# Kernel optimization log

Measured on AMD Instinct MI355X. Metric: run time of the kernel, lower is better.

The kernel has to match this reference:

```python
import jax, jax.numpy as jnp
import numpy as np
from jax import lax

N, E, F_NODE, F_EDGE, H, L = 100000, 3200000, 5, 2, 32, 18


def setup_inputs() -> dict:
    key = jax.random.key(0)
    ks = jax.random.split(key, 20)
    s = 0.1
    return {
        "x": jax.random.normal(ks[0], (N, F_NODE), dtype=jnp.float32),
        "edge_attr": jax.random.uniform(ks[1], (E, F_EDGE), dtype=jnp.float32),
        "edge_index": jax.random.randint(ks[2], (2, E), 0, N, dtype=jnp.int32),
        "Wn": jax.random.normal(ks[3], (F_NODE, H), dtype=jnp.float32) * s,
        "bn": jnp.zeros((H,), jnp.float32),
        "We": jax.random.normal(ks[4], (F_EDGE, H), dtype=jnp.float32) * s,
        "be": jnp.zeros((H,), jnp.float32),
        "ln_w": jax.random.normal(ks[5], (L, H, H), dtype=jnp.float32) * s,
        "ln_b": jnp.zeros((L, H), jnp.float32),
        "le_w": jax.random.normal(ks[6], (L, H, H), dtype=jnp.float32) * s,
        "le_b": jnp.zeros((L, H), jnp.float32),
        "lu_w": jax.random.normal(ks[7], (L, 2 * H, H), dtype=jnp.float32) * s,
        "lu_b": jnp.zeros((L, H), jnp.float32),
        "c1_w": jax.random.normal(ks[8], (H, H), dtype=jnp.float32) * s,
        "c1_b": jnp.zeros((H,), jnp.float32),
        "c2_w": jax.random.normal(ks[9], (H, 1), dtype=jnp.float32) * s,
        "c2_b": jnp.zeros((1,), jnp.float32),
    }


def reference(x, edge_attr, edge_index, Wn, bn, We, be,
              ln_w, ln_b, le_w, le_b, lu_w, lu_b, c1_w, c1_b, c2_w, c2_b):
    src, dst = edge_index[0], edge_index[1]
    n = x.shape[0]
    h = x @ Wn + bn                       # [N, H] node encoder
    ea = edge_attr @ We + be              # [E, H] edge encoder (shared by all layers)

    def layer(h, p):
        lnw, lnb, lew, leb, luw, lub = p
        ee = ea @ lew + leb               # [E, H] per-layer edge embedding
        xj = h[src]                       # gather source node states [E, H]
        msg = xj * (1.0 - ee) + ee * (xj @ lnw + lnb)
        agg = jax.ops.segment_sum(msg, dst, num_segments=n)  # scatter-add [N, H]
        out = jnp.concatenate([h, agg], axis=1) @ luw + lub
        return jax.nn.relu(out), None

    h, _ = lax.scan(layer, h, (ln_w, ln_b, le_w, le_b, lu_w, lu_b))
    logits = jax.nn.relu(h @ c1_w + c1_b) @ c2_w + c2_b   # classifier (dropout off at eval)
    return jax.nn.sigmoid(logits).squeeze(-1)             # [N]
```

## Files before the change

kernel.cpp:

```cpp
#include <hip/hip_runtime.h>
#include <hip/hip_bf16.h>
#include <hip/hip_fp8.h>
#include <math.h>

#define H 32
#define SCB 1024
#define S 6

__device__ __forceinline__ unsigned f2bf(float f) {
  unsigned u = __float_as_uint(f);
  return (u + 0x7fffu + ((u >> 16) & 1u)) >> 16;
}
__device__ __forceinline__ float bflo(unsigned p) { return __uint_as_float(p << 16); }
__device__ __forceinline__ float bfhi(unsigned p) { return __uint_as_float(p & 0xffff0000u); }

__device__ __forceinline__ unsigned f2q(float f) {
  __hip_fp8_e4m3 q(f);
  return (unsigned)q.__x;
}
__device__ __forceinline__ float q2f(unsigned b) {
  unsigned s = (b >> 7) & 1u, e = (b >> 3) & 15u, m = b & 7u;
  float vn = __uint_as_float((s << 31) | ((e + 120u) << 23) | (m << 20));
  float vs = __uint_as_float((s << 31) | 0x3f800000u) * ((float)(int)m * (1.0f / 512.0f));
  return (e == 0u) ? vs : vn;
}

template <bool HI>
__device__ __forceinline__ void cvt2(unsigned dw, float& x, float& u) {
#if __has_builtin(__builtin_amdgcn_cvt_pk_f32_fp8)
  typedef float f32x2 __attribute__((ext_vector_type(2)));
  f32x2 v = __builtin_amdgcn_cvt_pk_f32_fp8((int)dw, HI);
  x = v[0]; u = v[1];
#else
  unsigned b = HI ? (dw >> 16) : dw;
  x = q2f(b & 255u); u = q2f((b >> 8) & 255u);
#endif
}

__device__ __forceinline__ unsigned pack4(float x0, float u0, float x1, float u1) {
  return f2q(x0) | (f2q(u0) << 8) | (f2q(x1) << 16) | (f2q(u1) << 24);
}

__global__ void k_encode(const float* __restrict__ x, const float* __restrict__ Wn,
                         const float* __restrict__ bn, const float* __restrict__ lnw0,
                         const float* __restrict__ lnb0, float* __restrict__ h,
                         unsigned* __restrict__ pk, int n, int fnode) {
  __shared__ float sw[H * H];
  int tid = threadIdx.x;
  for (int i = tid; i < H * H; i += blockDim.x) sw[i] = lnw0[i];
  __syncthreads();
  int gid = blockIdx.x * blockDim.x + tid;
  int node = gid >> 5, c = gid & 31;
  if (node >= n) return;
  float acc = bn[c];
  for (int k = 0; k < fnode; ++k)
    acc = fmaf(x[node * fnode + k], Wn[k * H + c], acc);
  h[node * H + c] = acc;
  float t = lnb0[c];
#pragma unroll
  for (int k = 0; k < H; ++k)
    t = fmaf(__shfl(acc, k, 32), sw[k * H + c], t);
  unsigned w = f2q(acc) | (f2q(t - acc) << 8);
  unsigned dw = w | (__shfl_xor(w, 1, 32) << 16);
  if (!(c & 1)) pk[node * 16 + (c >> 1)] = dw;
}

__global__ void k_fold(const float* __restrict__ We, const float* __restrict__ be,
                       const float* __restrict__ lew, const float* __restrict__ leb,
                       float* __restrict__ W2, float* __restrict__ b2, int L) {
  int gid = blockIdx.x * blockDim.x + threadIdx.x;
  if (gid >= L * H) return;
  int l = gid >> 5, c = gid & 31;
  const float* lw = lew + (size_t)l * H * H;
  float a0 = 0.f, a1 = 0.f, bb = leb[l * H + c];
  for (int j = 0; j < H; ++j) {
    float w = lw[j * H + c];
    a0 = fmaf(We[j], w, a0);
    a1 = fmaf(We[H + j], w, a1);
    bb = fmaf(be[j], w, bb);
  }
  W2[l * 2 * H + c] = a0;
  W2[l * 2 * H + H + c] = a1;
  b2[l * H + c] = bb;
}

__global__ void k_hist(const int* __restrict__ dst, unsigned* __restrict__ cnt, int e) {
  int i = blockIdx.x * blockDim.x + threadIdx.x;
  if (i < e) atomicAdd(&cnt[dst[i]], 1u);
}

__global__ void k_scan1(const unsigned* __restrict__ cnt, unsigned* __restrict__ out,
                        unsigned* __restrict__ bsum, int n) {
  __shared__ unsigned s[SCB];
  int i = blockIdx.x * SCB + threadIdx.x;
  unsigned v = (i < n) ? cnt[i] : 0u;
  s[threadIdx.x] = v;
  __syncthreads();
  for (int off = 1; off < SCB; off <<= 1) {
    unsigned u = (threadIdx.x >= off) ? s[threadIdx.x - off] : 0u;
    __syncthreads();
    s[threadIdx.x] += u;
    __syncthreads();
  }
  if (i < n) out[i] = s[threadIdx.x] - v;
  if (threadIdx.x == SCB - 1) bsum[blockIdx.x] = s[SCB - 1];
}

__global__ void k_scan2(const unsigned* __restrict__ bsum, unsigned* __restrict__ boff,
                        unsigned* __restrict__ total_out, int nb) {
  __shared__ unsigned s[SCB];
  unsigned v = ((int)threadIdx.x < nb) ? bsum[threadIdx.x] : 0u;
  s[threadIdx.x] = v;
  __syncthreads();
  for (int off = 1; off < SCB; off <<= 1) {
    unsigned u = (threadIdx.x >= off) ? s[threadIdx.x - off] : 0u;
    __syncthreads();
    s[threadIdx.x] += u;
    __syncthreads();
  }
  if ((int)threadIdx.x < nb) boff[threadIdx.x] = s[threadIdx.x] - v;
  if (threadIdx.x == SCB - 1) *total_out = s[SCB - 1];
}

__global__ void k_scan3(unsigned* __restrict__ row_ptr, const unsigned* __restrict__ boff,
                        unsigned* __restrict__ fill, int n) {
  int i = blockIdx.x * blockDim.x + threadIdx.x;
  if (i >= n) return;
  unsigned v = row_ptr[i] + boff[i >> 10];
  row_ptr[i] = v;
  fill[i] = v;
}

__global__ void k_scatter(const int* __restrict__ src, const int* __restrict__ dst,
                          const float* __restrict__ ea, unsigned* __restrict__ fill,
                          unsigned long long* __restrict__ recs, int e) {
  int i = blockIdx.x * blockDim.x + threadIdx.x;
  if (i >= e) return;
  int d = dst[i];
  unsigned pos = atomicAdd(&fill[d], 1u);
  float2 a = ((const float2*)ea)[i];
  unsigned long long v = (unsigned long long)(unsigned)src[i] |
                         ((unsigned long long)(f2bf(a.x) | (f2bf(a.y) << 16)) << 32);
  __builtin_nontemporal_store(v, &recs[pos]);
}

__device__ __forceinline__ void edge_acc(float (&acc)[8], uint4 pv, unsigned attr, float v,
                                         const float (&w0v)[8], const float (&w1v)[8],
                                         const float (&bbv)[8]) {
  float a0 = bflo(attr), a1 = bfhi(attr);
  unsigned dws[4] = {pv.x, pv.y, pv.z, pv.w};
#pragma unroll
  for (int d = 0; d < 4; ++d) {
    float x0, u0, x1, u1;
    cvt2<false>(dws[d], x0, u0);
    cvt2<true>(dws[d], x1, u1);
    float e0 = fmaf(a0, w0v[2 * d], fmaf(a1, w1v[2 * d], bbv[2 * d]));
    float e1 = fmaf(a0, w0v[2 * d + 1], fmaf(a1, w1v[2 * d + 1], bbv[2 * d + 1]));
    acc[2 * d]     = fmaf(v, fmaf(e0, u0, x0), acc[2 * d]);
    acc[2 * d + 1] = fmaf(v, fmaf(e1, u1, x1), acc[2 * d + 1]);
  }
}

__global__ void __launch_bounds__(256) k_gather(
    const unsigned* __restrict__ pk, const unsigned* __restrict__ row_ptr,
    const unsigned long long* __restrict__ recs, const float* __restrict__ W2l,
    const float* __restrict__ b2l, float* __restrict__ agg, int n, int e) {
  int tid = threadIdx.x;
  int lane = tid & 63;
  int wv = blockIdx.x * 4 + (tid >> 6);
  int n0 = wv * S;
  if (n0 >= n) return;
  int sub = lane & 3;
  unsigned eoff = (unsigned)(lane >> 2);
  float w0v[8], w1v[8], bbv[8];
#pragma unroll
  for (int j = 0; j < 8; ++j) {
    int ch = sub * 8 + j;
    w0v[j] = W2l[ch]; w1v[j] = W2l[H + ch]; bbv[j] = b2l[ch];
  }
  unsigned rp[S + 1];
#pragma unroll
  for (int i = 0; i <= S; ++i) {
    int idx = n0 + i;
    rp[i] = row_ptr[idx < n ? idx : n];
  }
  unsigned b0[S], b1[S], rr[S];
  unsigned R = 0;
#pragma unroll
  for (int s = 0; s < S; ++s) {
    b0[s] = rp[s]; b1[s] = rp[s + 1];
    rr[s] = (b1[s] - b0[s] + 15u) >> 4;
    R = rr[s] > R ? rr[s] : R;
  }
  float acc[S][8] = {};
  const uint4* pk4 = (const uint4*)pk;
  unsigned emax = (unsigned)(e - 1);
  unsigned long long cur[S], nxt[S];
#pragma unroll
  for (int s = 0; s < S; ++s) {
    unsigned ix = b0[s] + eoff;
    unsigned cl = (ix < b1[s]) ? ix : b0[s];
    cl = cl < emax ? cl : emax;
    cur[s] = __builtin_nontemporal_load(&recs[cl]);
  }
  for (unsigned r = 0; r < R; ++r) {
    uint4 pv[S];
#pragma unroll
    for (int s = 0; s < S; ++s)
      if (r < rr[s]) pv[s] = pk4[(size_t)(unsigned)cur[s] * 4 + sub];
#pragma unroll
    for (int s = 0; s < S; ++s) {
      nxt[s] = cur[s];
      if (r + 1 < rr[s]) {
        unsigned ix = b0[s] + (r + 1) * 16u + eoff;
        unsigned cl = (ix < b1[s]) ? ix : b0[s];
        cl = cl < emax ? cl : emax;
        nxt[s] = __builtin_nontemporal_load(&recs[cl]);
      }
    }
    unsigned rb = r << 4;
#pragma unroll
    for (int s = 0; s < S; ++s)
      if (r < rr[s]) {
        float v = (b0[s] + rb + eoff < b1[s]) ? 1.f : 0.f;
        edge_acc(acc[s], pv[s], (unsigned)(cur[s] >> 32), v, w0v, w1v, bbv);
      }
#pragma unroll
    for (int s = 0; s < S; ++s) cur[s] = nxt[s];
  }
#pragma unroll
  for (int s = 0; s < S; ++s)
#pragma unroll
    for (int j = 0; j < 8; ++j) {
      acc[s][j] += __shfl_xor(acc[s][j], 4, 64);
      acc[s][j] += __shfl_xor(acc[s][j], 8, 64);
      acc[s][j] += __shfl_xor(acc[s][j], 16, 64);
      acc[s][j] += __shfl_xor(acc[s][j], 32, 64);
    }
  if (lane < 4) {
#pragma unroll
    for (int s = 0; s < S; ++s) {
      if (n0 + s < n) {
        float4* o = (float4*)&agg[(size_t)(n0 + s) * H + lane * 8];
        o[0] = make_float4(acc[s][0], acc[s][1], acc[s][2], acc[s][3]);
        o[1] = make_float4(acc[s][4], acc[s][5], acc[s][6], acc[s][7]);
      }
    }
  }
}

__global__ void __launch_bounds__(256) k_update(
    const float* __restrict__ h, const float* __restrict__ agg,
    const float* __restrict__ luw, const float* __restrict__ lub,
    const float* __restrict__ lnw, const float* __restrict__ lnb,
    float* __restrict__ hout, unsigned* __restrict__ pkout, int n) {
  int node = blockIdx.x * blockDim.x + threadIdx.x;
  if (node >= n) return;
  float hr[H], ar[H];
  const float4* h4 = (const float4*)(h + (size_t)node * H);
  const float4* a4 = (const float4*)(agg + (size_t)node * H);
#pragma unroll
  for (int q = 0; q < 8; ++q) {
    float4 v = h4[q];
    hr[4 * q] = v.x; hr[4 * q + 1] = v.y; hr[4 * q + 2] = v.z; hr[4 * q + 3] = v.w;
  }
#pragma unroll
  for (int q = 0; q < 8; ++q) {
    float4 v = a4[q];
    ar[4 * q] = v.x; ar[4 * q + 1] = v.y; ar[4 * q + 2] = v.z; ar[4 * q + 3] = v.w;
  }
  float o[H];
#pragma unroll
  for (int c = 0; c < H; ++c) o[c] = lub[c];
#pragma unroll
  for (int k = 0; k < H; ++k)
#pragma unroll
    for (int c = 0; c < H; ++c)
      o[c] = fmaf(hr[k], luw[k * H + c], o[c]);
#pragma unroll
  for (int k = 0; k < H; ++k)
#pragma unroll
    for (int c = 0; c < H; ++c)
      o[c] = fmaf(ar[k], luw[(H + k) * H + c], o[c]);
#pragma unroll
  for (int c = 0; c < H; ++c) o[c] = fmaxf(o[c], 0.f);
  float4* ho = (float4*)(hout + (size_t)node * H);
#pragma unroll
  for (int q = 0; q < 8; ++q)
    ho[q] = make_float4(o[4 * q], o[4 * q + 1], o[4 * q + 2], o[4 * q + 3]);
  if (pkout) {
    float t[H];
#pragma unroll
    for (int c = 0; c < H; ++c) t[c] = lnb[c];
#pragma unroll
    for (int k = 0; k < H; ++k)
#pragma unroll
      for (int c = 0; c < H; ++c)
        t[c] = fmaf(o[k], lnw[k * H + c], t[c]);
    unsigned dws[16];
#pragma unroll
    for (int d = 0; d < 16; ++d)
      dws[d] = pack4(o[2 * d], t[2 * d] - o[2 * d],
                     o[2 * d + 1], t[2 * d + 1] - o[2 * d + 1]);
    uint4* po = (uint4*)(pkout + (size_t)node * 16);
#pragma unroll
    for (int q = 0; q < 4; ++q)
      po[q] = make_uint4(dws[4 * q], dws[4 * q + 1], dws[4 * q + 2], dws[4 * q + 3]);
  }
}

__global__ void k_cls(const float* __restrict__ h, const float* __restrict__ c1w,
                      const float* __restrict__ c1b, const float* __restrict__ c2w,
                      const float* __restrict__ c2b, float* __restrict__ out, int n) {
  __shared__ float sw[H * H];
  int tid = threadIdx.x;
  for (int i = tid; i < H * H; i += blockDim.x) sw[i] = c1w[i];
  __syncthreads();
  int gid = blockIdx.x * blockDim.x + tid;
  int node = gid >> 5, c = gid & 31;
  if (node >= n) return;
  float hv = h[node * H + c];
  float z = c1b[c];
#pragma unroll
  for (int k = 0; k < H; ++k)
    z = fmaf(__shfl(hv, k, 32), sw[k * H + c], z);
  z = fmaxf(z, 0.f);
  float r = z * c2w[c];
#pragma unroll
  for (int m = 16; m >= 1; m >>= 1)
    r += __shfl_xor(r, m, 32);
  if (c == 0) out[node] = 1.f / (1.f + expf(-(r + c2b[0])));
}

extern "C" void kernel_launch(void* const* d_in, const int* in_sizes, int n_in,
                              void* d_out, int out_size, void* d_ws, size_t ws_size,
                              hipStream_t stream) {
  const float* x         = (const float*)d_in[0];
  const float* edge_attr = (const float*)d_in[1];
  const int*   edge_index= (const int*)d_in[2];
  const float* Wn        = (const float*)d_in[3];
  const float* bn        = (const float*)d_in[4];
  const float* We        = (const float*)d_in[5];
  const float* be        = (const float*)d_in[6];
  const float* ln_w      = (const float*)d_in[7];
  const float* ln_b      = (const float*)d_in[8];
  const float* le_w      = (const float*)d_in[9];
  const float* le_b      = (const float*)d_in[10];
  const float* lu_w      = (const float*)d_in[11];
  const float* lu_b      = (const float*)d_in[12];
  const float* c1w       = (const float*)d_in[13];
  const float* c1b       = (const float*)d_in[14];
  const float* c2w       = (const float*)d_in[15];
  const float* c2b       = (const float*)d_in[16];

  const int N_ = in_sizes[0] / 5;
  const int E_ = in_sizes[1] / 2;
  const int L_ = in_sizes[7] / (H * H);
  const int* src = edge_index;
  const int* dst = edge_index + E_;

  char* ws = (char*)d_ws;
  size_t off = 0;
  auto alloc = [&](size_t bytes) -> void* {
    void* p = ws + off;
    off = (off + bytes + 255) & ~(size_t)255;
    return p;
  };
  float*              hA      = (float*)alloc((size_t)N_ * H * 4);
  float*              hB      = (float*)alloc((size_t)N_ * H * 4);
  unsigned*           pkA     = (unsigned*)alloc((size_t)N_ * 16 * 4);
  unsigned*           pkB     = (unsigned*)alloc((size_t)N_ * 16 * 4);
  float*              agg     = (float*)alloc((size_t)N_ * H * 4);
  unsigned*           row_ptr = (unsigned*)alloc((size_t)(N_ + 1) * 4);
  unsigned*           fill    = (unsigned*)alloc((size_t)N_ * 4);
  unsigned long long* recs    = (unsigned long long*)alloc((size_t)E_ * 8);
  float*              W2      = (float*)alloc((size_t)L_ * 2 * H * 4);
  float*              b2      = (float*)alloc((size_t)L_ * H * 4);
  unsigned*           bsum    = (unsigned*)alloc((size_t)SCB * 4);
  unsigned*           boff    = (unsigned*)alloc((size_t)SCB * 4);

  const int tb = 256;
  const int nb = (N_ + SCB - 1) / SCB;
  hipMemsetAsync(fill, 0, (size_t)N_ * 4, stream);
  k_encode<<<(N_ * 32 + tb - 1) / tb, tb, 0, stream>>>(x, Wn, bn, ln_w, ln_b, hA, pkA, N_, 5);
  k_fold<<<(L_ * H + 63) / 64, 64, 0, stream>>>(We, be, le_w, le_b, W2, b2, L_);
  k_hist<<<(E_ + tb - 1) / tb, tb, 0, stream>>>(dst, fill, E_);
  k_scan1<<<nb, SCB, 0, stream>>>(fill, row_ptr, bsum, N_);
  k_scan2<<<1, SCB, 0, stream>>>(bsum, boff, row_ptr + N_, nb);
  k_scan3<<<(N_ + tb - 1) / tb, tb, 0, stream>>>(row_ptr, boff, fill, N_);
  k_scatter<<<(E_ + tb - 1) / tb, tb, 0, stream>>>(src, dst, edge_attr, fill, recs, E_);

  float* hc = hA;  float* hn = hB;
  unsigned* pc = pkA; unsigned* pn = pkB;
  const int gblocks = (N_ + 4 * S - 1) / (4 * S);
  for (int l = 0; l < L_; ++l) {
    bool last = (l == L_ - 1);
    k_gather<<<gblocks, 256, 0, stream>>>(
        pc, row_ptr, recs, W2 + l * 2 * H, b2 + l * H, agg, N_, E_);
    k_update<<<(N_ + tb - 1) / tb, tb, 0, stream>>>(
        hc, agg, lu_w + (size_t)l * 2 * H * H, lu_b + (size_t)l * H,
        last ? nullptr : ln_w + (size_t)(l + 1) * H * H,
        last ? nullptr : ln_b + (size_t)(l + 1) * H,
        hn, last ? nullptr : pn, N_);
    float* tf = hc; hc = hn; hn = tf;
    unsigned* tp = pc; pc = pn; pn = tp;
  }
  k_cls<<<(N_ * 32 + tb - 1) / tb, tb, 0, stream>>>(hc, c1w, c1b, c2w, c2b, (float*)d_out, N_);
}
```

Baseline: 2.260 ms.

## Partition CSR scatter by XCD and deepen gather prefetch pipeline

The CSR scatter kernel becomes a persistent kernel in which each block reads its XCC hardware ID and first handles destination ranges owned by its own XCD. Chunks are handed out through per-range atomic work queues, so the atomics and record writes for a destination range tend to stay in one XCD's L2 instead of bouncing across dies. The gather kernel gets a two-deep prefetch of edge records and one-ahead prefetch of packed node features, with fewer nodes per wave (S 6→4) to offset the extra registers, and it drops the nontemporal hints. The cost is that each edge chunk's dst array is re-read 8 times in the scatter, and the gather uses more registers per node slot.

```diff
diff --git a/kernel.cpp b/kernel.cpp
--- a/kernel.cpp
+++ b/kernel.cpp
@@ -5,7 +5,9 @@
 
 #define H 32
 #define SCB 1024
-#define S 6
+#define S 4
+#define NXCD 8
+#define SCCH 4096
 
 __device__ __forceinline__ unsigned f2bf(float f) {
   unsigned u = __float_as_uint(f);
@@ -131,17 +133,37 @@
   fill[i] = v;
 }
 
-__global__ void k_scatter(const int* __restrict__ src, const int* __restrict__ dst,
-                          const float* __restrict__ ea, unsigned* __restrict__ fill,
-                          unsigned long long* __restrict__ recs, int e) {
-  int i = blockIdx.x * blockDim.x + threadIdx.x;
-  if (i >= e) return;
-  int d = dst[i];
-  unsigned pos = atomicAdd(&fill[d], 1u);
-  float2 a = ((const float2*)ea)[i];
-  unsigned long long v = (unsigned long long)(unsigned)src[i] |
-                         ((unsigned long long)(f2bf(a.x) | (f2bf(a.y) << 16)) << 32);
-  __builtin_nontemporal_store(v, &recs[pos]);
+__global__ void __launch_bounds__(256) k_scatter(
+    const int* __restrict__ src, const int* __restrict__ dst,
+    const float* __restrict__ ea, unsigned* __restrict__ fill,
+    uint2* __restrict__ recs, unsigned* __restrict__ q, int e, int n) {
+  __shared__ unsigned sh_chunk;
+  unsigned xcc;
+  asm volatile("s_getreg_b32 %0, hwreg(HW_REG_XCC_ID)" : "=s"(xcc));
+  xcc &= (NXCD - 1);
+  const unsigned nchunks = (unsigned)((e + SCCH - 1) / SCCH);
+  for (int pass = 0; pass < NXCD; ++pass) {
+    unsigned qi = (xcc + (unsigned)pass) & (NXCD - 1);
+    unsigned lo = (unsigned)((unsigned long long)n * qi / NXCD);
+    unsigned hi = (unsigned)((unsigned long long)n * (qi + 1) / NXCD);
+    for (;;) {
+      if (threadIdx.x == 0) sh_chunk = atomicAdd(&q[qi], 1u);
+      __syncthreads();
+      unsigned c = sh_chunk;
+      __syncthreads();
+      if (c >= nchunks) break;
+      int base = (int)(c * SCCH);
+      int end = base + SCCH; end = end < e ? end : e;
+      for (int i = base + (int)threadIdx.x; i < end; i += 256) {
+        unsigned d = (unsigned)dst[i];
+        if (d >= lo && d < hi) {
+          unsigned pos = atomicAdd(&fill[d], 1u);
+          float2 a = ((const float2*)ea)[i];
+          recs[pos] = make_uint2((unsigned)src[i], f2bf(a.x) | (f2bf(a.y) << 16));
+        }
+      }
+    }
+  }
 }
 
 __device__ __forceinline__ void edge_acc(float (&acc)[8], uint4 pv, unsigned attr, float v,
@@ -163,7 +185,7 @@
 
 __global__ void __launch_bounds__(256) k_gather(
     const unsigned* __restrict__ pk, const unsigned* __restrict__ row_ptr,
-    const unsigned long long* __restrict__ recs, const float* __restrict__ W2l,
+    const uint2* __restrict__ recs, const float* __restrict__ W2l,
     const float* __restrict__ b2l, float* __restrict__ agg, int n, int e) {
   int tid = threadIdx.x;
   int lane = tid & 63;
@@ -195,27 +217,39 @@
   float acc[S][8] = {};
   const uint4* pk4 = (const uint4*)pk;
   unsigned emax = (unsigned)(e - 1);
-  unsigned long long cur[S], nxt[S];
+  uint2 cur[S], nxt[S];
+  uint4 pcur[S];
 #pragma unroll
   for (int s = 0; s < S; ++s) {
     unsigned ix = b0[s] + eoff;
     unsigned cl = (ix < b1[s]) ? ix : b0[s];
-    cl = cl < emax ? cl : emax;
-    cur[s] = __builtin_nontemporal_load(&recs[cl]);
-  }
+    cur[s] = recs[cl < emax ? cl : emax];
+  }
+#pragma unroll
+  for (int s = 0; s < S; ++s) {
+    nxt[s] = cur[s];
+    if (rr[s] > 1) {
+      unsigned ix = b0[s] + 16u + eoff;
+      unsigned cl = (ix < b1[s]) ? ix : b0[s];
+      nxt[s] = recs[cl < emax ? cl : emax];
+    }
+  }
+#pragma unroll
+  for (int s = 0; s < S; ++s)
+    if (rr[s] > 0) pcur[s] = pk4[(size_t)cur[s].x * 4 + sub];
   for (unsigned r = 0; r < R; ++r) {
-    uint4 pv[S];
+    uint4 pnxt[S];
 #pragma unroll
     for (int s = 0; s < S; ++s)
-      if (r < rr[s]) pv[s] = pk4[(size_t)(unsigned)cur[s] * 4 + sub];
+      if (r + 1 < rr[s]) pnxt[s] = pk4[(size_t)nxt[s].x * 4 + sub];
+    uint2 fut[S];
 #pragma unroll
     for (int s = 0; s < S; ++s) {
-      nxt[s] = cur[s];
-      if (r + 1 < rr[s]) {
-        unsigned ix = b0[s] + (r + 1) * 16u + eoff;
+      fut[s] = nxt[s];
+      if (r + 2 < rr[s]) {
+        unsigned ix = b0[s] + (r + 2) * 16u + eoff;
         unsigned cl = (ix < b1[s]) ? ix : b0[s];
-        cl = cl < emax ? cl : emax;
-        nxt[s] = __builtin_nontemporal_load(&recs[cl]);
+        fut[s] = recs[cl < emax ? cl : emax];
       }
     }
     unsigned rb = r << 4;
@@ -223,10 +257,12 @@
     for (int s = 0; s < S; ++s)
       if (r < rr[s]) {
         float v = (b0[s] + rb + eoff < b1[s]) ? 1.f : 0.f;
-        edge_acc(acc[s], pv[s], (unsigned)(cur[s] >> 32), v, w0v, w1v, bbv);
+        edge_acc(acc[s], pcur[s], cur[s].y, v, w0v, w1v, bbv);
       }
 #pragma unroll
-    for (int s = 0; s < S; ++s) cur[s] = nxt[s];
+    for (int s = 0; s < S; ++s) {
+      cur[s] = nxt[s]; nxt[s] = fut[s]; pcur[s] = pnxt[s];
+    }
   }
 #pragma unroll
   for (int s = 0; s < S; ++s)
@@ -366,29 +402,31 @@
     off = (off + bytes + 255) & ~(size_t)255;
     return p;
   };
-  float*              hA      = (float*)alloc((size_t)N_ * H * 4);
-  float*              hB      = (float*)alloc((size_t)N_ * H * 4);
-  unsigned*           pkA     = (unsigned*)alloc((size_t)N_ * 16 * 4);
-  unsigned*           pkB     = (unsigned*)alloc((size_t)N_ * 16 * 4);
-  float*              agg     = (float*)alloc((size_t)N_ * H * 4);
-  unsigned*           row_ptr = (unsigned*)alloc((size_t)(N_ + 1) * 4);
-  unsigned*           fill    = (unsigned*)alloc((size_t)N_ * 4);
-  unsigned long long* recs    = (unsigned long long*)alloc((size_t)E_ * 8);
-  float*              W2      = (float*)alloc((size_t)L_ * 2 * H * 4);
-  float*              b2      = (float*)alloc((size_t)L_ * H * 4);
-  unsigned*           bsum    = (unsigned*)alloc((size_t)SCB * 4);
-  unsigned*           boff    = (unsigned*)alloc((size_t)SCB * 4);
+  float*    hA      = (float*)alloc((size_t)N_ * H * 4);
+  float*    hB      = (float*)alloc((size_t)N_ * H * 4);
+  unsigned* pkA     = (unsigned*)alloc((size_t)N_ * 16 * 4);
+  unsigned* pkB     = (unsigned*)alloc((size_t)N_ * 16 * 4);
+  float*    agg     = (float*)alloc((size_t)N_ * H * 4);
+  unsigned* row_ptr = (unsigned*)alloc((size_t)(N_ + 1) * 4);
+  unsigned* fill    = (unsigned*)alloc((size_t)N_ * 4);
+  uint2*    recs    = (uint2*)alloc((size_t)E_ * 8);
+  float*    W2      = (float*)alloc((size_t)L_ * 2 * H * 4);
+  float*    b2      = (float*)alloc((size_t)L_ * H * 4);
+  unsigned* bsum    = (unsigned*)alloc((size_t)SCB * 4);
+  unsigned* boff    = (unsigned*)alloc((size_t)SCB * 4);
+  unsigned* qq      = (unsigned*)alloc((size_t)NXCD * 4);
 
   const int tb = 256;
   const int nb = (N_ + SCB - 1) / SCB;
   hipMemsetAsync(fill, 0, (size_t)N_ * 4, stream);
+  hipMemsetAsync(qq, 0, (size_t)NXCD * 4, stream);
   k_encode<<<(N_ * 32 + tb - 1) / tb, tb, 0, stream>>>(x, Wn, bn, ln_w, ln_b, hA, pkA, N_, 5);
   k_fold<<<(L_ * H + 63) / 64, 64, 0, stream>>>(We, be, le_w, le_b, W2, b2, L_);
   k_hist<<<(E_ + tb - 1) / tb, tb, 0, stream>>>(dst, fill, E_);
   k_scan1<<<nb, SCB, 0, stream>>>(fill, row_ptr, bsum, N_);
   k_scan2<<<1, SCB, 0, stream>>>(bsum, boff, row_ptr + N_, nb);
   k_scan3<<<(N_ + tb - 1) / tb, tb, 0, stream>>>(row_ptr, boff, fill, N_);
-  k_scatter<<<(E_ + tb - 1) / tb, tb, 0, stream>>>(src, dst, edge_attr, fill, recs, E_);
+  k_scatter<<<1024, 256, 0, stream>>>(src, dst, edge_attr, fill, recs, qq, E_, N_);
 
   float* hc = hA;  float* hn = hB;
   unsigned* pc = pkA; unsigned* pn = pkB;
```

Result: faster. 2.176 ms (-3.7%).

## Split packed node features into two channel halves gathered in separate passes

Applied to the files above, without the earlier changes.

The packed fp8 node table is stored as two half-width arrays of 16 channels each, and each layer runs the gather kernel twice, once per half. Each half-table is 3.2MB instead of 6.4MB, so a pass is more likely to stay in cache during the random source gathers. The cost is reading the edge records twice per layer and launching an extra kernel. Nodes per wave drop from 6 to 4, and the edge records lose their nontemporal load and store hints, so they may now stay cached between the two passes.

```diff
diff --git a/kernel.cpp b/kernel.cpp
--- a/kernel.cpp
+++ b/kernel.cpp
@@ -5,7 +5,7 @@
 
 #define H 32
 #define SCB 1024
-#define S 6
+#define S 4
 
 __device__ __forceinline__ unsigned f2bf(float f) {
   unsigned u = __float_as_uint(f);
@@ -44,7 +44,8 @@
 __global__ void k_encode(const float* __restrict__ x, const float* __restrict__ Wn,
                          const float* __restrict__ bn, const float* __restrict__ lnw0,
                          const float* __restrict__ lnb0, float* __restrict__ h,
-                         unsigned* __restrict__ pk, int n, int fnode) {
+                         unsigned* __restrict__ pk0, unsigned* __restrict__ pk1,
+                         int n, int fnode) {
   __shared__ float sw[H * H];
   int tid = threadIdx.x;
   for (int i = tid; i < H * H; i += blockDim.x) sw[i] = lnw0[i];
@@ -62,7 +63,10 @@
     t = fmaf(__shfl(acc, k, 32), sw[k * H + c], t);
   unsigned w = f2q(acc) | (f2q(t - acc) << 8);
   unsigned dw = w | (__shfl_xor(w, 1, 32) << 16);
-  if (!(c & 1)) pk[node * 16 + (c >> 1)] = dw;
+  if (!(c & 1)) {
+    unsigned* ph = (c < 16) ? pk0 : pk1;
+    ph[node * 8 + ((c & 15) >> 1)] = dw;
+  }
 }
 
 __global__ void k_fold(const float* __restrict__ We, const float* __restrict__ be,
@@ -133,15 +137,13 @@
 
 __global__ void k_scatter(const int* __restrict__ src, const int* __restrict__ dst,
                           const float* __restrict__ ea, unsigned* __restrict__ fill,
-                          unsigned long long* __restrict__ recs, int e) {
+                          uint2* __restrict__ recs, int e) {
   int i = blockIdx.x * blockDim.x + threadIdx.x;
   if (i >= e) return;
   int d = dst[i];
   unsigned pos = atomicAdd(&fill[d], 1u);
   float2 a = ((const float2*)ea)[i];
-  unsigned long long v = (unsigned long long)(unsigned)src[i] |
-                         ((unsigned long long)(f2bf(a.x) | (f2bf(a.y) << 16)) << 32);
-  __builtin_nontemporal_store(v, &recs[pos]);
+  recs[pos] = make_uint2((unsigned)src[i], f2bf(a.x) | (f2bf(a.y) << 16));
 }
 
 __device__ __forceinline__ void edge_acc(float (&acc)[8], uint4 pv, unsigned attr, float v,
@@ -162,20 +164,20 @@
 }
 
 __global__ void __launch_bounds__(256) k_gather(
-    const unsigned* __restrict__ pk, const unsigned* __restrict__ row_ptr,
-    const unsigned long long* __restrict__ recs, const float* __restrict__ W2l,
-    const float* __restrict__ b2l, float* __restrict__ agg, int n, int e) {
+    const unsigned* __restrict__ pkh, const unsigned* __restrict__ row_ptr,
+    const uint2* __restrict__ recs, const float* __restrict__ W2l,
+    const float* __restrict__ b2l, int co, float* __restrict__ agg, int n, int e) {
   int tid = threadIdx.x;
   int lane = tid & 63;
   int wv = blockIdx.x * 4 + (tid >> 6);
   int n0 = wv * S;
   if (n0 >= n) return;
-  int sub = lane & 3;
-  unsigned eoff = (unsigned)(lane >> 2);
+  int sub = lane & 1;
+  unsigned eoff = (unsigned)(lane >> 1);
   float w0v[8], w1v[8], bbv[8];
 #pragma unroll
   for (int j = 0; j < 8; ++j) {
-    int ch = sub * 8 + j;
+    int ch = co + sub * 8 + j;
     w0v[j] = W2l[ch]; w1v[j] = W2l[H + ch]; bbv[j] = b2l[ch];
   }
   unsigned rp[S + 1];
@@ -189,41 +191,39 @@
 #pragma unroll
   for (int s = 0; s < S; ++s) {
     b0[s] = rp[s]; b1[s] = rp[s + 1];
-    rr[s] = (b1[s] - b0[s] + 15u) >> 4;
+    rr[s] = (b1[s] - b0[s] + 31u) >> 5;
     R = rr[s] > R ? rr[s] : R;
   }
   float acc[S][8] = {};
-  const uint4* pk4 = (const uint4*)pk;
+  const uint4* pk4 = (const uint4*)pkh;
   unsigned emax = (unsigned)(e - 1);
-  unsigned long long cur[S], nxt[S];
+  uint2 cur[S], nxt[S];
 #pragma unroll
   for (int s = 0; s < S; ++s) {
     unsigned ix = b0[s] + eoff;
     unsigned cl = (ix < b1[s]) ? ix : b0[s];
-    cl = cl < emax ? cl : emax;
-    cur[s] = __builtin_nontemporal_load(&recs[cl]);
+    cur[s] = recs[cl < emax ? cl : emax];
   }
   for (unsigned r = 0; r < R; ++r) {
     uint4 pv[S];
 #pragma unroll
     for (int s = 0; s < S; ++s)
-      if (r < rr[s]) pv[s] = pk4[(size_t)(unsigned)cur[s] * 4 + sub];
+      if (r < rr[s]) pv[s] = pk4[(size_t)cur[s].x * 2 + sub];
 #pragma unroll
     for (int s = 0; s < S; ++s) {
       nxt[s] = cur[s];
       if (r + 1 < rr[s]) {
-        unsigned ix = b0[s] + (r + 1) * 16u + eoff;
+        unsigned ix = b0[s] + (r + 1) * 32u + eoff;
         unsigned cl = (ix < b1[s]) ? ix : b0[s];
-        cl = cl < emax ? cl : emax;
-        nxt[s] = __builtin_nontemporal_load(&recs[cl]);
+        nxt[s] = recs[cl < emax ? cl : emax];
       }
     }
-    unsigned rb = r << 4;
+    unsigned rb = r << 5;
 #pragma unroll
     for (int s = 0; s < S; ++s)
       if (r < rr[s]) {
         float v = (b0[s] + rb + eoff < b1[s]) ? 1.f : 0.f;
-        edge_acc(acc[s], pv[s], (unsigned)(cur[s] >> 32), v, w0v, w1v, bbv);
+        edge_acc(acc[s], pv[s], cur[s].y, v, w0v, w1v, bbv);
       }
 #pragma unroll
     for (int s = 0; s < S; ++s) cur[s] = nxt[s];
@@ -232,16 +232,17 @@
   for (int s = 0; s < S; ++s)
 #pragma unroll
     for (int j = 0; j < 8; ++j) {
+      acc[s][j] += __shfl_xor(acc[s][j], 2, 64);
       acc[s][j] += __shfl_xor(acc[s][j], 4, 64);
       acc[s][j] += __shfl_xor(acc[s][j], 8, 64);
       acc[s][j] += __shfl_xor(acc[s][j], 16, 64);
       acc[s][j] += __shfl_xor(acc[s][j], 32, 64);
     }
-  if (lane < 4) {
+  if (lane < 2) {
 #pragma unroll
     for (int s = 0; s < S; ++s) {
       if (n0 + s < n) {
-        float4* o = (float4*)&agg[(size_t)(n0 + s) * H + lane * 8];
+        float4* o = (float4*)&agg[(size_t)(n0 + s) * H + co + lane * 8];
         o[0] = make_float4(acc[s][0], acc[s][1], acc[s][2], acc[s][3]);
         o[1] = make_float4(acc[s][4], acc[s][5], acc[s][6], acc[s][7]);
       }
@@ -253,7 +254,8 @@
     const float* __restrict__ h, const float* __restrict__ agg,
     const float* __restrict__ luw, const float* __restrict__ lub,
     const float* __restrict__ lnw, const float* __restrict__ lnb,
-    float* __restrict__ hout, unsigned* __restrict__ pkout, int n) {
+    float* __restrict__ hout, unsigned* __restrict__ pk0,
+    unsigned* __restrict__ pk1, int n) {
   int node = blockIdx.x * blockDim.x + threadIdx.x;
   if (node >= n) return;
   float hr[H], ar[H];
@@ -288,7 +290,7 @@
 #pragma unroll
   for (int q = 0; q < 8; ++q)
     ho[q] = make_float4(o[4 * q], o[4 * q + 1], o[4 * q + 2], o[4 * q + 3]);
-  if (pkout) {
+  if (pk0) {
     float t[H];
 #pragma unroll
     for (int c = 0; c < H; ++c) t[c] = lnb[c];
@@ -302,10 +304,12 @@
     for (int d = 0; d < 16; ++d)
       dws[d] = pack4(o[2 * d], t[2 * d] - o[2 * d],
                      o[2 * d + 1], t[2 * d + 1] - o[2 * d + 1]);
-    uint4* po = (uint4*)(pkout + (size_t)node * 16);
-#pragma unroll
-    for (int q = 0; q < 4; ++q)
-      po[q] = make_uint4(dws[4 * q], dws[4 * q + 1], dws[4 * q + 2], dws[4 * q + 3]);
+    uint4* p0 = (uint4*)(pk0 + (size_t)node * 8);
+    p0[0] = make_uint4(dws[0], dws[1], dws[2], dws[3]);
+    p0[1] = make_uint4(dws[4], dws[5], dws[6], dws[7]);
+    uint4* p1 = (uint4*)(pk1 + (size_t)node * 8);
+    p1[0] = make_uint4(dws[8], dws[9], dws[10], dws[11]);
+    p1[1] = make_uint4(dws[12], dws[13], dws[14], dws[15]);
   }
 }
 
@@ -366,23 +370,25 @@
     off = (off + bytes + 255) & ~(size_t)255;
     return p;
   };
-  float*              hA      = (float*)alloc((size_t)N_ * H * 4);
-  float*              hB      = (float*)alloc((size_t)N_ * H * 4);
-  unsigned*           pkA     = (unsigned*)alloc((size_t)N_ * 16 * 4);
-  unsigned*           pkB     = (unsigned*)alloc((size_t)N_ * 16 * 4);
-  float*              agg     = (float*)alloc((size_t)N_ * H * 4);
-  unsigned*           row_ptr = (unsigned*)alloc((size_t)(N_ + 1) * 4);
-  unsigned*           fill    = (unsigned*)alloc((size_t)N_ * 4);
-  unsigned long long* recs    = (unsigned long long*)alloc((size_t)E_ * 8);
-  float*              W2      = (float*)alloc((size_t)L_ * 2 * H * 4);
-  float*              b2      = (float*)alloc((size_t)L_ * H * 4);
-  unsigned*           bsum    = (unsigned*)alloc((size_t)SCB * 4);
-  unsigned*           boff    = (unsigned*)alloc((size_t)SCB * 4);
+  float*    hA      = (float*)alloc((size_t)N_ * H * 4);
+  float*    hB      = (float*)alloc((size_t)N_ * H * 4);
+  unsigned* pkA0    = (unsigned*)alloc((size_t)N_ * 8 * 4);
+  unsigned* pkA1    = (unsigned*)alloc((size_t)N_ * 8 * 4);
+  unsigned* pkB0    = (unsigned*)alloc((size_t)N_ * 8 * 4);
+  unsigned* pkB1    = (unsigned*)alloc((size_t)N_ * 8 * 4);
+  float*    agg     = (float*)alloc((size_t)N_ * H * 4);
+  unsigned* row_ptr = (unsigned*)alloc((size_t)(N_ + 1) * 4);
+  unsigned* fill    = (unsigned*)alloc((size_t)N_ * 4);
+  uint2*    recs    = (uint2*)alloc((size_t)E_ * 8);
+  float*    W2      = (float*)alloc((size_t)L_ * 2 * H * 4);
+  float*    b2      = (float*)alloc((size_t)L_ * H * 4);
+  unsigned* bsum    = (unsigned*)alloc((size_t)SCB * 4);
+  unsigned* boff    = (unsigned*)alloc((size_t)SCB * 4);
 
   const int tb = 256;
   const int nb = (N_ + SCB - 1) / SCB;
   hipMemsetAsync(fill, 0, (size_t)N_ * 4, stream);
-  k_encode<<<(N_ * 32 + tb - 1) / tb, tb, 0, stream>>>(x, Wn, bn, ln_w, ln_b, hA, pkA, N_, 5);
+  k_encode<<<(N_ * 32 + tb - 1) / tb, tb, 0, stream>>>(x, Wn, bn, ln_w, ln_b, hA, pkA0, pkA1, N_, 5);
   k_fold<<<(L_ * H + 63) / 64, 64, 0, stream>>>(We, be, le_w, le_b, W2, b2, L_);
   k_hist<<<(E_ + tb - 1) / tb, tb, 0, stream>>>(dst, fill, E_);
   k_scan1<<<nb, SCB, 0, stream>>>(fill, row_ptr, bsum, N_);
@@ -391,19 +397,23 @@
   k_scatter<<<(E_ + tb - 1) / tb, tb, 0, stream>>>(src, dst, edge_attr, fill, recs, E_);
 
   float* hc = hA;  float* hn = hB;
-  unsigned* pc = pkA; unsigned* pn = pkB;
+  unsigned* pc0 = pkA0; unsigned* pc1 = pkA1;
+  unsigned* pn0 = pkB0; unsigned* pn1 = pkB1;
   const int gblocks = (N_ + 4 * S - 1) / (4 * S);
   for (int l = 0; l < L_; ++l) {
     bool last = (l == L_ - 1);
-    k_gather<<<gblocks, 256, 0, stream>>>(
-        pc, row_ptr, recs, W2 + l * 2 * H, b2 + l * H, agg, N_, E_);
+    const float* w2l = W2 + l * 2 * H;
+    const float* b2l = b2 + l * H;
+    k_gather<<<gblocks, 256, 0, stream>>>(pc0, row_ptr, recs, w2l, b2l, 0, agg, N_, E_);
+    k_gather<<<gblocks, 256, 0, stream>>>(pc1, row_ptr, recs, w2l, b2l, 16, agg, N_, E_);
     k_update<<<(N_ + tb - 1) / tb, tb, 0, stream>>>(
         hc, agg, lu_w + (size_t)l * 2 * H * H, lu_b + (size_t)l * H,
         last ? nullptr : ln_w + (size_t)(l + 1) * H * H,
         last ? nullptr : ln_b + (size_t)(l + 1) * H,
-        hn, last ? nullptr : pn, N_);
+        hn, last ? nullptr : pn0, last ? nullptr : pn1, N_);
     float* tf = hc; hc = hn; hn = tf;
-    unsigned* tp = pc; pc = pn; pn = tp;
+    unsigned* t0 = pc0; pc0 = pn0; pn0 = t0;
+    unsigned* t1 = pc1; pc1 = pn1; pn1 = t1;
   }
   k_cls<<<(N_ * 32 + tb - 1) / tb, tb, 0, stream>>>(hc, c1w, c1b, c2w, c2b, (float*)d_out, N_);
 }
```

New measurement: 2.721 ms. +20.4%, slower.

## Sort nodes by in-degree for balanced per-wave gather workloads

Applied to the files above, without the earlier changes.

Adds a one-time counting sort of nodes by in-degree (histogram, scan, scatter into an order array). The gather kernel then processes the nodes of each wave in that order, so the S nodes sharing a wave have similar edge counts and fewer lanes idle while the longest row finishes. S drops from 6 to 4 and the nontemporal record loads and stores become plain uint2 accesses. Each gather now does an extra indirection through the order array, and its agg writes are scattered instead of contiguous.

```diff
diff --git a/kernel.cpp b/kernel.cpp
--- a/kernel.cpp
+++ b/kernel.cpp
@@ -5,7 +5,8 @@
 
 #define H 32
 #define SCB 1024
-#define S 6
+#define S 4
+#define DB 1024
 
 __device__ __forceinline__ unsigned f2bf(float f) {
   unsigned u = __float_as_uint(f);
@@ -131,17 +132,39 @@
   fill[i] = v;
 }
 
+__global__ void k_dhist(const unsigned* __restrict__ row_ptr, unsigned* __restrict__ dcnt,
+                        int n) {
+  int i = blockIdx.x * blockDim.x + threadIdx.x;
+  if (i >= n) return;
+  unsigned d = row_ptr[i + 1] - row_ptr[i];
+  d = d < (DB - 1) ? d : (DB - 1);
+  atomicAdd(&dcnt[d], 1u);
+}
+
+__global__ void k_copy(const unsigned* __restrict__ a, unsigned* __restrict__ b, int n) {
+  int i = blockIdx.x * blockDim.x + threadIdx.x;
+  if (i < n) b[i] = a[i];
+}
+
+__global__ void k_dscatter(const unsigned* __restrict__ row_ptr, unsigned* __restrict__ dfill,
+                           unsigned* __restrict__ order, int n) {
+  int i = blockIdx.x * blockDim.x + threadIdx.x;
+  if (i >= n) return;
+  unsigned d = row_ptr[i + 1] - row_ptr[i];
+  d = d < (DB - 1) ? d : (DB - 1);
+  unsigned pos = atomicAdd(&dfill[d], 1u);
+  order[pos] = (unsigned)i;
+}
+
 __global__ void k_scatter(const int* __restrict__ src, const int* __restrict__ dst,
                           const float* __restrict__ ea, unsigned* __restrict__ fill,
-                          unsigned long long* __restrict__ recs, int e) {
+                          uint2* __restrict__ recs, int e) {
   int i = blockIdx.x * blockDim.x + threadIdx.x;
   if (i >= e) return;
   int d = dst[i];
   unsigned pos = atomicAdd(&fill[d], 1u);
   float2 a = ((const float2*)ea)[i];
-  unsigned long long v = (unsigned long long)(unsigned)src[i] |
-                         ((unsigned long long)(f2bf(a.x) | (f2bf(a.y) << 16)) << 32);
-  __builtin_nontemporal_store(v, &recs[pos]);
+  recs[pos] = make_uint2((unsigned)src[i], f2bf(a.x) | (f2bf(a.y) << 16));
 }
 
 __device__ __forceinline__ void edge_acc(float (&acc)[8], uint4 pv, unsigned attr, float v,
@@ -163,8 +186,9 @@
 
 __global__ void __launch_bounds__(256) k_gather(
     const unsigned* __restrict__ pk, const unsigned* __restrict__ row_ptr,
-    const unsigned long long* __restrict__ recs, const float* __restrict__ W2l,
-    const float* __restrict__ b2l, float* __restrict__ agg, int n, int e) {
+    const unsigned* __restrict__ order, const uint2* __restrict__ recs,
+    const float* __restrict__ W2l, const float* __restrict__ b2l,
+    float* __restrict__ agg, int n, int e) {
   int tid = threadIdx.x;
   int lane = tid & 63;
   int wv = blockIdx.x * 4 + (tid >> 6);
@@ -178,44 +202,39 @@
     int ch = sub * 8 + j;
     w0v[j] = W2l[ch]; w1v[j] = W2l[H + ch]; bbv[j] = b2l[ch];
   }
-  unsigned rp[S + 1];
-#pragma unroll
-  for (int i = 0; i <= S; ++i) {
-    int idx = n0 + i;
-    rp[i] = row_ptr[idx < n ? idx : n];
-  }
-  unsigned b0[S], b1[S], rr[S];
+  unsigned nd[S], b0[S], b1[S], rr[S];
   unsigned R = 0;
 #pragma unroll
   for (int s = 0; s < S; ++s) {
-    b0[s] = rp[s]; b1[s] = rp[s + 1];
+    int oi = n0 + s;
+    nd[s] = (oi < n) ? order[oi] : 0u;
+    b0[s] = row_ptr[nd[s]];
+    b1[s] = (oi < n) ? row_ptr[nd[s] + 1] : b0[s];
     rr[s] = (b1[s] - b0[s] + 15u) >> 4;
     R = rr[s] > R ? rr[s] : R;
   }
   float acc[S][8] = {};
   const uint4* pk4 = (const uint4*)pk;
   unsigned emax = (unsigned)(e - 1);
-  unsigned long long cur[S], nxt[S];
+  uint2 cur[S], nxt[S];
 #pragma unroll
   for (int s = 0; s < S; ++s) {
     unsigned ix = b0[s] + eoff;
     unsigned cl = (ix < b1[s]) ? ix : b0[s];
-    cl = cl < emax ? cl : emax;
-    cur[s] = __builtin_nontemporal_load(&recs[cl]);
+    cur[s] = recs[cl < emax ? cl : emax];
   }
   for (unsigned r = 0; r < R; ++r) {
     uint4 pv[S];
 #pragma unroll
     for (int s = 0; s < S; ++s)
-      if (r < rr[s]) pv[s] = pk4[(size_t)(unsigned)cur[s] * 4 + sub];
+      if (r < rr[s]) pv[s] = pk4[(size_t)cur[s].x * 4 + sub];
 #pragma unroll
     for (int s = 0; s < S; ++s) {
       nxt[s] = cur[s];
       if (r + 1 < rr[s]) {
         unsigned ix = b0[s] + (r + 1) * 16u + eoff;
         unsigned cl = (ix < b1[s]) ? ix : b0[s];
-        cl = cl < emax ? cl : emax;
-        nxt[s] = __builtin_nontemporal_load(&recs[cl]);
+        nxt[s] = recs[cl < emax ? cl : emax];
       }
     }
     unsigned rb = r << 4;
@@ -223,7 +242,7 @@
     for (int s = 0; s < S; ++s)
       if (r < rr[s]) {
         float v = (b0[s] + rb + eoff < b1[s]) ? 1.f : 0.f;
-        edge_acc(acc[s], pv[s], (unsigned)(cur[s] >> 32), v, w0v, w1v, bbv);
+        edge_acc(acc[s], pv[s], cur[s].y, v, w0v, w1v, bbv);
       }
 #pragma unroll
     for (int s = 0; s < S; ++s) cur[s] = nxt[s];
@@ -241,7 +260,7 @@
 #pragma unroll
     for (int s = 0; s < S; ++s) {
       if (n0 + s < n) {
-        float4* o = (float4*)&agg[(size_t)(n0 + s) * H + lane * 8];
+        float4* o = (float4*)&agg[(size_t)nd[s] * H + lane * 8];
         o[0] = make_float4(acc[s][0], acc[s][1], acc[s][2], acc[s][3]);
         o[1] = make_float4(acc[s][4], acc[s][5], acc[s][6], acc[s][7]);
       }
@@ -366,22 +385,27 @@
     off = (off + bytes + 255) & ~(size_t)255;
     return p;
   };
-  float*              hA      = (float*)alloc((size_t)N_ * H * 4);
-  float*              hB      = (float*)alloc((size_t)N_ * H * 4);
-  unsigned*           pkA     = (unsigned*)alloc((size_t)N_ * 16 * 4);
-  unsigned*           pkB     = (unsigned*)alloc((size_t)N_ * 16 * 4);
-  float*              agg     = (float*)alloc((size_t)N_ * H * 4);
-  unsigned*           row_ptr = (unsigned*)alloc((size_t)(N_ + 1) * 4);
-  unsigned*           fill    = (unsigned*)alloc((size_t)N_ * 4);
-  unsigned long long* recs    = (unsigned long long*)alloc((size_t)E_ * 8);
-  float*              W2      = (float*)alloc((size_t)L_ * 2 * H * 4);
-  float*              b2      = (float*)alloc((size_t)L_ * H * 4);
-  unsigned*           bsum    = (unsigned*)alloc((size_t)SCB * 4);
-  unsigned*           boff    = (unsigned*)alloc((size_t)SCB * 4);
+  float*    hA      = (float*)alloc((size_t)N_ * H * 4);
+  float*    hB      = (float*)alloc((size_t)N_ * H * 4);
+  unsigned* pkA     = (unsigned*)alloc((size_t)N_ * 16 * 4);
+  unsigned* pkB     = (unsigned*)alloc((size_t)N_ * 16 * 4);
+  float*    agg     = (float*)alloc((size_t)N_ * H * 4);
+  unsigned* row_ptr = (unsigned*)alloc((size_t)(N_ + 1) * 4);
+  unsigned* fill    = (unsigned*)alloc((size_t)N_ * 4);
+  unsigned* order   = (unsigned*)alloc((size_t)N_ * 4);
+  uint2*    recs    = (uint2*)alloc((size_t)E_ * 8);
+  float*    W2      = (float*)alloc((size_t)L_ * 2 * H * 4);
+  float*    b2      = (float*)alloc((size_t)L_ * H * 4);
+  unsigned* bsum    = (unsigned*)alloc((size_t)SCB * 4);
+  unsigned* boff    = (unsigned*)alloc((size_t)SCB * 4);
+  unsigned* dcnt    = (unsigned*)alloc((size_t)DB * 4);
+  unsigned* doff    = (unsigned*)alloc((size_t)DB * 4);
+  unsigned* dtot    = (unsigned*)alloc(4);
 
   const int tb = 256;
   const int nb = (N_ + SCB - 1) / SCB;
   hipMemsetAsync(fill, 0, (size_t)N_ * 4, stream);
+  hipMemsetAsync(dcnt, 0, (size_t)DB * 4, stream);
   k_encode<<<(N_ * 32 + tb - 1) / tb, tb, 0, stream>>>(x, Wn, bn, ln_w, ln_b, hA, pkA, N_, 5);
   k_fold<<<(L_ * H + 63) / 64, 64, 0, stream>>>(We, be, le_w, le_b, W2, b2, L_);
   k_hist<<<(E_ + tb - 1) / tb, tb, 0, stream>>>(dst, fill, E_);
@@ -389,6 +413,10 @@
   k_scan2<<<1, SCB, 0, stream>>>(bsum, boff, row_ptr + N_, nb);
   k_scan3<<<(N_ + tb - 1) / tb, tb, 0, stream>>>(row_ptr, boff, fill, N_);
   k_scatter<<<(E_ + tb - 1) / tb, tb, 0, stream>>>(src, dst, edge_attr, fill, recs, E_);
+  k_dhist<<<(N_ + tb - 1) / tb, tb, 0, stream>>>(row_ptr, dcnt, N_);
+  k_scan2<<<1, SCB, 0, stream>>>(dcnt, doff, dtot, DB);
+  k_copy<<<(DB + tb - 1) / tb, tb, 0, stream>>>(doff, dcnt, DB);
+  k_dscatter<<<(N_ + tb - 1) / tb, tb, 0, stream>>>(row_ptr, dcnt, order, N_);
 
   float* hc = hA;  float* hn = hB;
   unsigned* pc = pkA; unsigned* pn = pkB;
@@ -396,7 +424,7 @@
   for (int l = 0; l < L_; ++l) {
     bool last = (l == L_ - 1);
     k_gather<<<gblocks, 256, 0, stream>>>(
-        pc, row_ptr, recs, W2 + l * 2 * H, b2 + l * H, agg, N_, E_);
+        pc, row_ptr, order, recs, W2 + l * 2 * H, b2 + l * H, agg, N_, E_);
     k_update<<<(N_ + tb - 1) / tb, tb, 0, stream>>>(
         hc, agg, lu_w + (size_t)l * 2 * H * H, lu_b + (size_t)l * H,
         last ? nullptr : ln_w + (size_t)(l + 1) * H * H,
```

New measurement: 2.484 ms. 9.9% more time.
